# Kernel tuning notes

Hardware: AMD Instinct MI355X
Metric: run time of the kernel (lower is better)

Reference implementation:

```python
import jax, jax.numpy as jnp
import numpy as np

G_NUM, K_DEG = 3, 3  # grid intervals, spline order (module defaults)
LN_EPS = 1e-5


def _bspline_basis(x, grid, k):
    """Cox-de Boor B-spline basis. x: [N, D], grid: [D, G+2k+1] -> [N, D, G+k]."""
    xg = x[:, :, None]                      # [N, D, 1]
    g = grid[None, :, :]                    # [1, D, M]
    B = ((xg >= g[..., :-1]) & (xg < g[..., 1:])).astype(x.dtype)  # degree 0
    for d in range(1, k + 1):
        left = (xg - g[..., :-(d + 1)]) / (g[..., d:-1] - g[..., :-(d + 1)])
        right = (g[..., d + 1:] - xg) / (g[..., d + 1:] - g[..., 1:-d])
        B = left * B[..., :-1] + right * B[..., 1:]
    return B                                # [N, D, G+k]


def _kan_layer(x, grid, coef, scale_base, scale_sp, node_scale, node_bias):
    # spline branch: fold per-edge scale_sp into coef, contract basis without
    # materializing the [N, in, out] per-edge tensor
    basis = _bspline_basis(x, grid, K_DEG)              # [N, in, G+k]
    coef_eff = coef * scale_sp[..., None]               # [in, out, G+k]
    y = jnp.einsum('nib,iob->no', basis, coef_eff)      # spline sum over edges
    y = y + jax.nn.silu(x) @ scale_base                 # residual base function
    return node_scale * y + node_bias                   # per-node affine


def setup_inputs() -> dict:
    key = jax.random.key(0)
    ks = jax.random.split(key, 12)
    B, S = 16, 1024
    D0, D1, D2 = 256, 512, 256
    nb = G_NUM + K_DEG  # num basis fns = 6
    h = 2.0 / G_NUM
    knots = np.arange(-K_DEG, G_NUM + K_DEG + 1) * h - 1.0  # [G+2k+1]=10, range [-3,3]
    grid1 = jnp.asarray(np.tile(knots, (D0, 1)), jnp.float32)
    grid2 = jnp.asarray(np.tile(knots, (D1, 1)), jnp.float32)
    inp = {
        'x': jax.random.normal(ks[0], (B, S, D0), jnp.float32),
        'grid1': grid1,
        'coef1': jax.random.normal(ks[1], (D0, D1, nb), jnp.float32) * 0.1,
        'scale_base1': jax.random.normal(ks[2], (D0, D1), jnp.float32) / np.sqrt(D0),
        'scale_sp1': jnp.ones((D0, D1), jnp.float32),
        'node_scale1': jnp.ones((D1,), jnp.float32),
        'node_bias1': jnp.zeros((D1,), jnp.float32),
        'grid2': grid2,
        'coef2': jax.random.normal(ks[3], (D1, D2, nb), jnp.float32) * 0.1,
        'scale_base2': jax.random.normal(ks[4], (D1, D2), jnp.float32) / np.sqrt(D1),
        'scale_sp2': jnp.ones((D1, D2), jnp.float32),
        'node_scale2': jnp.ones((D2,), jnp.float32),
        'node_bias2': jnp.zeros((D2,), jnp.float32),
        'ln_gamma': jnp.ones((D2,), jnp.float32),
        'ln_beta': jnp.zeros((D2,), jnp.float32),
    }
    return inp


def reference(x, grid1, coef1, scale_base1, scale_sp1, node_scale1, node_bias1,
              grid2, coef2, scale_base2, scale_sp2, node_scale2, node_bias2,
              ln_gamma, ln_beta):
    b, s, d = x.shape
    residual = x  # start_dim == final_dim -> residual path active
    h = x.reshape(-1, d)
    h = _kan_layer(h, grid1, coef1, scale_base1, scale_sp1, node_scale1, node_bias1)
    h = _kan_layer(h, grid2, coef2, scale_base2, scale_sp2, node_scale2, node_bias2)
    h = h.reshape(b, s, -1)
    h = h + residual
    # LayerNorm over last dim
    mu = jnp.mean(h, axis=-1, keepdims=True)
    var = jnp.mean((h - mu) ** 2, axis=-1, keepdims=True)
    h = (h - mu) * jax.lax.rsqrt(var + LN_EPS) * ln_gamma + ln_beta
    # torch nn.GELU default is exact (erf) variant
    return jax.nn.gelu(h, approximate=False)
```

## Files before the change

kernel.cpp:

```cpp
#include <hip/hip_runtime.h>
#include <cstdint>
#include <cstddef>

using f16   = _Float16;
using half4 = __attribute__((ext_vector_type(4))) _Float16;
using half8 = __attribute__((ext_vector_type(8))) _Float16;
using f32x4 = __attribute__((ext_vector_type(4))) float;
using ull   = unsigned long long;

#define DINL __device__ __forceinline__

DINL void gload_lds16(const void* gptr, void* lptr) {
  __builtin_amdgcn_global_load_lds(
      reinterpret_cast<const __attribute__((address_space(1))) uint32_t*>(
          reinterpret_cast<uintptr_t>(gptr)),
      reinterpret_cast<__attribute__((address_space(3))) uint32_t*>(
          reinterpret_cast<uintptr_t>(lptr)),
      16, 0, 0);
}

DINL unsigned pkh(float a, float b) {
  unsigned short ha = __builtin_bit_cast(unsigned short, (f16)a);
  unsigned short hb = __builtin_bit_cast(unsigned short, (f16)b);
  return (unsigned)ha | ((unsigned)hb << 16);
}

struct U4 { unsigned x, y, z, w; };

DINL U4 expand_pack(float x) {
  float xs = (x + 3.0f) * 1.5f;
  float mf = floorf(xs);
  int   m  = (int)mf;
  float u = xs - mf, u2 = u * u, u3 = u2 * u, um = 1.0f - u;
  float p3 = u3 * (1.0f / 6.0f);
  float p2 = (1.0f + 3.0f * (u + u2 - u3)) * (1.0f / 6.0f);
  float p1 = (4.0f - 6.0f * u2 + 3.0f * u3) * (1.0f / 6.0f);
  float p0 = um * um * um * (1.0f / 6.0f);
  ull P = (ull)pkh(p0, p1) | ((ull)pkh(p2, p3) << 32);
  if ((unsigned)m > 8u) P = 0;
  int s    = m * 16 - 48;
  int sneg = min(63, max(0, -s));
  int spos = min(63, max(0, s));
  int shi2 = min(63, max(0, s - 64));
  ull rlo = (s < 0) ? (P >> sneg) : ((s < 64) ? (P << spos) : 0ull);
  ull rhi = (s < 0) ? 0ull
                    : ((s < 64) ? ((P >> (63 - spos)) >> 1) : (P << shi2));
  float sil = x / (1.0f + __expf(-x));
  U4 r;
  r.x = (unsigned)rlo;
  r.y = (unsigned)(rlo >> 32);
  r.z = (unsigned)rhi;
  r.w = pkh(sil, 0.0f);
  return r;
}

__global__ __launch_bounds__(256)
void prep_w_kernel(const float* __restrict__ coef, const float* __restrict__ ssp,
                   const float* __restrict__ sb, f16* __restrict__ Wt,
                   int Din, int Dout) {
  int idx = blockIdx.x * 256 + threadIdx.x;
  if (idx >= Din * Dout) return;
  int n = idx / Din;
  int d = idx - n * Din;
  float s = ssp[(size_t)d * Dout + n];
  const float* c = coef + ((size_t)d * Dout + n) * 6;
  half8 wv;
#pragma unroll
  for (int b = 0; b < 6; ++b) wv[b] = (f16)(c[b] * s);
  wv[6] = (f16)sb[(size_t)d * Dout + n];
  wv[7] = (f16)0.0f;
  int dp = (d & ~7) | ((d & 7) ^ (n & 7));
  *reinterpret_cast<half8*>(Wt + ((size_t)n * Din + dp) * 8) = wv;
}

template <bool BIAS, typename TIN, typename TOUT>
__global__ __launch_bounds__(512, 4)
void kan_gemm(const TIN* __restrict__ X, int ldx,
              const f16* __restrict__ Wt, int ldw,
              const float* __restrict__ nscale, const float* __restrict__ nbias,
              int N, TOUT* __restrict__ Out, int nsteps) {
  __shared__ alignas(16) f16 A0[64 * 64];
  __shared__ alignas(16) f16 A1[64 * 64];
  __shared__ alignas(16) f16 B0[256 * 64];
  __shared__ alignas(16) f16 B1[256 * 64];

  const int tid  = threadIdx.x;
  const int w    = tid >> 6;
  const int lane = tid & 63;
  const int l15  = lane & 15, l7 = lane & 7, hi = lane >> 4;
  const int wm   = w >> 2, wn = w & 3;
  const int m0   = blockIdx.y * 64;
  const int n0   = blockIdx.x * 256;
  const int dim0 = blockIdx.z * (nsteps * 8);
  TOUT* outz = Out + (size_t)blockIdx.z * ((size_t)gridDim.y * 64) * N;

  const int ar = tid >> 3, ad = tid & 7;
  const TIN* asrc = X + (size_t)(m0 + ar) * ldx + dim0 + ad;
  const int aoff = ar * 64 + 8 * (ad ^ (ar & 7));

  const f16* wb[4];
  int ldsb[4];
#pragma unroll
  for (int q = 0; q < 4; ++q) {
    int c   = tid + q * 512;
    wb[q]   = Wt + (size_t)(n0 + (c >> 3)) * ldw + (size_t)dim0 * 8 + (c & 7) * 8;
    ldsb[q] = c * 8;
  }

  f32x4 acc[2][4] = {};

  auto stageB = [&](f16* buf, int k0) {
#pragma unroll
    for (int q = 0; q < 4; ++q) gload_lds16(wb[q] + k0, buf + ldsb[q]);
  };

  auto compute = [&](const f16* bA, const f16* bB) {
    __builtin_amdgcn_s_setprio(1);
#pragma unroll
    for (int kk = 0; kk < 2; ++kk) {
      const int sl = kk * 4 + hi;
      half8 av[2], bv[4];
#pragma unroll
      for (int i = 0; i < 2; ++i)
        av[i] = *reinterpret_cast<const half8*>(
            bA + (wm * 32 + i * 16 + l15) * 64 + 8 * (sl ^ l7));
#pragma unroll
      for (int j = 0; j < 4; ++j)
        bv[j] = *reinterpret_cast<const half8*>(
            bB + (wn * 64 + j * 16 + l15) * 64 + 8 * (sl ^ l7));
#pragma unroll
      for (int i = 0; i < 2; ++i)
#pragma unroll
        for (int j = 0; j < 4; ++j)
          acc[i][j] = __builtin_amdgcn_mfma_f32_16x16x32_f16(av[i], bv[j], acc[i][j], 0, 0, 0);
    }
    __builtin_amdgcn_s_setprio(0);
  };

  auto writeA = [&](f16* buf, U4 e) {
    *reinterpret_cast<U4*>(buf + aoff) = e;
  };

  {
    float xa = (float)asrc[0];
    stageB(B0, 0);
    writeA(A0, expand_pack(xa));
  }
  float xn = (float)asrc[8];
  __syncthreads();

  const TIN* ap = asrc + 16;
  const int npairs = (nsteps - 2) >> 1;
  int k = 64;
  for (int p = 0; p < npairs; ++p) {
    stageB(B1, k);
    float xa2 = (float)ap[0];
    compute(A0, B0);
    writeA(A1, expand_pack(xn));
    __syncthreads();
    stageB(B0, k + 64);
    xn = (float)ap[8];
    compute(A1, B1);
    writeA(A0, expand_pack(xa2));
    __syncthreads();
    ap += 16;
    k  += 128;
  }

  stageB(B1, k);
  compute(A0, B0);
  writeA(A1, expand_pack(xn));
  __syncthreads();
  compute(A1, B1);

#pragma unroll
  for (int j = 0; j < 4; ++j) {
    int col   = n0 + wn * 64 + j * 16 + l15;
    float nsv = nscale[col];
    float nbv = BIAS ? nbias[col] : 0.0f;
#pragma unroll
    for (int i = 0; i < 2; ++i) {
      int rb = m0 + wm * 32 + i * 16 + hi * 4;
#pragma unroll
      for (int r = 0; r < 4; ++r)
        outz[(size_t)(rb + r) * N + col] = (TOUT)(nsv * acc[i][j][r] + nbv);
    }
  }
}

__global__ __launch_bounds__(256)
void ln_gelu_kernel(const f16* __restrict__ P0, const f16* __restrict__ P1,
                    const float* __restrict__ X,  const float* __restrict__ nb2,
                    const float* __restrict__ gamma, const float* __restrict__ beta,
                    float* __restrict__ out, int rows) {
  int row  = blockIdx.x * 4 + (threadIdx.x >> 6);
  int lane = threadIdx.x & 63;
  if (row >= rows) return;
  const half4  a4 = *reinterpret_cast<const half4*>(P0 + (size_t)row * 256 + lane * 4);
  const half4  b4 = *reinterpret_cast<const half4*>(P1 + (size_t)row * 256 + lane * 4);
  const float4 xr = *reinterpret_cast<const float4*>(X  + (size_t)row * 256 + lane * 4);
  const float4 nb = *reinterpret_cast<const float4*>(nb2 + lane * 4);
  const float4 g  = *reinterpret_cast<const float4*>(gamma + lane * 4);
  const float4 be = *reinterpret_cast<const float4*>(beta + lane * 4);
  float h[4];
#pragma unroll
  for (int j = 0; j < 4; ++j)
    h[j] = (float)a4[j] + (float)b4[j] + (&nb.x)[j] + (&xr.x)[j];
  float s = h[0] + h[1] + h[2] + h[3];
#pragma unroll
  for (int o = 32; o >= 1; o >>= 1) s += __shfl_xor(s, o);
  float mu = s * (1.0f / 256.0f);
  float vs = 0.f;
#pragma unroll
  for (int j = 0; j < 4; ++j) { float d = h[j] - mu; vs += d * d; }
#pragma unroll
  for (int o = 32; o >= 1; o >>= 1) vs += __shfl_xor(vs, o);
  float inv = rsqrtf(vs * (1.0f / 256.0f) + 1e-5f);
  float o4[4];
#pragma unroll
  for (int j = 0; j < 4; ++j) {
    float v = (h[j] - mu) * inv * (&g.x)[j] + (&be.x)[j];
    o4[j] = 0.5f * v * (1.0f + erff(v * 0.70710678118654752f));
  }
  *reinterpret_cast<float4*>(out + (size_t)row * 256 + lane * 4) =
      make_float4(o4[0], o4[1], o4[2], o4[3]);
}

extern "C" void kernel_launch(void* const* d_in, const int* in_sizes, int n_in,
                              void* d_out, int out_size, void* d_ws, size_t ws_size,
                              hipStream_t stream) {
  (void)in_sizes; (void)n_in; (void)out_size; (void)ws_size;
  const float* x     = (const float*)d_in[0];
  const float* coef1 = (const float*)d_in[2];
  const float* sb1   = (const float*)d_in[3];
  const float* ssp1  = (const float*)d_in[4];
  const float* ns1   = (const float*)d_in[5];
  const float* nb1   = (const float*)d_in[6];
  const float* coef2 = (const float*)d_in[8];
  const float* sb2   = (const float*)d_in[9];
  const float* ssp2  = (const float*)d_in[10];
  const float* ns2   = (const float*)d_in[11];
  const float* nb2   = (const float*)d_in[12];
  const float* lgam  = (const float*)d_in[13];
  const float* lbet  = (const float*)d_in[14];
  float* out = (float*)d_out;

  const int Ntok = 16 * 1024;
  const int D0 = 256, D1 = 512, D2 = 256;

  char* ws    = (char*)d_ws;
  f16*  h1    = (f16*)ws;
  size_t off  = (size_t)Ntok * D1 * sizeof(f16);
  f16*  part  = (f16*)(ws + off);
  off += (size_t)2 * Ntok * D2 * sizeof(f16);
  f16* Wt1 = (f16*)(ws + off);
  off += (size_t)D1 * D0 * 8 * sizeof(f16);
  f16* Wt2 = (f16*)(ws + off);

  prep_w_kernel<<<(D0 * D1 + 255) / 256, 256, 0, stream>>>(coef1, ssp1, sb1, Wt1, D0, D1);
  prep_w_kernel<<<(D1 * D2 + 255) / 256, 256, 0, stream>>>(coef2, ssp2, sb2, Wt2, D1, D2);

  kan_gemm<true, float, f16><<<dim3(D1 / 256, Ntok / 64, 1), 512, 0, stream>>>(
      x, D0, Wt1, D0 * 8, ns1, nb1, D1, h1, D0 / 8);

  kan_gemm<false, f16, f16><<<dim3(D2 / 256, Ntok / 64, 2), 512, 0, stream>>>(
      h1, D1, Wt2, D1 * 8, ns2, nullptr, D2, part, D1 / 16);

  ln_gelu_kernel<<<Ntok / 4, 256, 0, stream>>>(
      part, part + (size_t)Ntok * D2, x, nb2, lgam, lbet, out, Ntok);
}
```

Before: 118.6 us.

## Load weight fragments directly from global into registers, drop B LDS staging

The GEMM no longer stages weight tiles through LDS via global_load_lds. Each wave now reads its B fragments straight from global memory into registers, with the weight layout left unswizzled to match. Blocks shrink to 4 waves of 256 threads, and each wave covers the full 64 rows and 64 columns (a 4x4 MFMA tile). This cuts LDS use and barrier traffic, but B loads are no longer shared across waves through LDS and their latency is exposed right before the MFMAs with no prefetch.

```diff
diff --git a/kernel.cpp b/kernel.cpp
--- a/kernel.cpp
+++ b/kernel.cpp
@@ -9,15 +9,6 @@
 using ull   = unsigned long long;
 
 #define DINL __device__ __forceinline__
-
-DINL void gload_lds16(const void* gptr, void* lptr) {
-  __builtin_amdgcn_global_load_lds(
-      reinterpret_cast<const __attribute__((address_space(1))) uint32_t*>(
-          reinterpret_cast<uintptr_t>(gptr)),
-      reinterpret_cast<__attribute__((address_space(3))) uint32_t*>(
-          reinterpret_cast<uintptr_t>(lptr)),
-      16, 0, 0);
-}
 
 DINL unsigned pkh(float a, float b) {
   unsigned short ha = __builtin_bit_cast(unsigned short, (f16)a);
@@ -69,118 +60,126 @@
   for (int b = 0; b < 6; ++b) wv[b] = (f16)(c[b] * s);
   wv[6] = (f16)sb[(size_t)d * Dout + n];
   wv[7] = (f16)0.0f;
-  int dp = (d & ~7) | ((d & 7) ^ (n & 7));
-  *reinterpret_cast<half8*>(Wt + ((size_t)n * Din + dp) * 8) = wv;
+  *reinterpret_cast<half8*>(Wt + ((size_t)n * Din + d) * 8) = wv;
 }
 
 template <bool BIAS, typename TIN, typename TOUT>
-__global__ __launch_bounds__(512, 4)
+__global__ __launch_bounds__(256, 2)
 void kan_gemm(const TIN* __restrict__ X, int ldx,
               const f16* __restrict__ Wt, int ldw,
               const float* __restrict__ nscale, const float* __restrict__ nbias,
               int N, TOUT* __restrict__ Out, int nsteps) {
   __shared__ alignas(16) f16 A0[64 * 64];
   __shared__ alignas(16) f16 A1[64 * 64];
-  __shared__ alignas(16) f16 B0[256 * 64];
-  __shared__ alignas(16) f16 B1[256 * 64];
 
   const int tid  = threadIdx.x;
   const int w    = tid >> 6;
   const int lane = tid & 63;
   const int l15  = lane & 15, l7 = lane & 7, hi = lane >> 4;
-  const int wm   = w >> 2, wn = w & 3;
   const int m0   = blockIdx.y * 64;
   const int n0   = blockIdx.x * 256;
   const int dim0 = blockIdx.z * (nsteps * 8);
   TOUT* outz = Out + (size_t)blockIdx.z * ((size_t)gridDim.y * 64) * N;
 
   const int ar = tid >> 3, ad = tid & 7;
-  const TIN* asrc = X + (size_t)(m0 + ar) * ldx + dim0 + ad;
-  const int aoff = ar * 64 + 8 * (ad ^ (ar & 7));
-
-  const f16* wb[4];
-  int ldsb[4];
-#pragma unroll
-  for (int q = 0; q < 4; ++q) {
-    int c   = tid + q * 512;
-    wb[q]   = Wt + (size_t)(n0 + (c >> 3)) * ldw + (size_t)dim0 * 8 + (c & 7) * 8;
-    ldsb[q] = c * 8;
-  }
-
-  f32x4 acc[2][4] = {};
-
-  auto stageB = [&](f16* buf, int k0) {
-#pragma unroll
-    for (int q = 0; q < 4; ++q) gload_lds16(wb[q] + k0, buf + ldsb[q]);
-  };
-
-  auto compute = [&](const f16* bA, const f16* bB) {
+  const TIN* asrc0 = X + (size_t)(m0 + ar) * ldx + dim0 + ad;
+  const TIN* asrc1 = asrc0 + (size_t)32 * ldx;
+  const int aoff0 = ar * 64 + 8 * (ad ^ (ar & 7));
+  const int aoff1 = aoff0 + 32 * 64;
+
+  const f16* bbase = Wt + (size_t)(n0 + w * 64 + l15) * ldw + (size_t)dim0 * 8 + hi * 8;
+  const size_t bj = (size_t)16 * ldw;
+
+  f32x4 acc[4][4] = {};
+
+  auto compute = [&](const f16* bA, const half8* bv) {
     __builtin_amdgcn_s_setprio(1);
 #pragma unroll
     for (int kk = 0; kk < 2; ++kk) {
       const int sl = kk * 4 + hi;
-      half8 av[2], bv[4];
-#pragma unroll
-      for (int i = 0; i < 2; ++i)
+      half8 av[4];
+#pragma unroll
+      for (int i = 0; i < 4; ++i)
         av[i] = *reinterpret_cast<const half8*>(
-            bA + (wm * 32 + i * 16 + l15) * 64 + 8 * (sl ^ l7));
-#pragma unroll
-      for (int j = 0; j < 4; ++j)
-        bv[j] = *reinterpret_cast<const half8*>(
-            bB + (wn * 64 + j * 16 + l15) * 64 + 8 * (sl ^ l7));
-#pragma unroll
-      for (int i = 0; i < 2; ++i)
+            bA + (i * 16 + l15) * 64 + 8 * (sl ^ l7));
+#pragma unroll
+      for (int i = 0; i < 4; ++i)
 #pragma unroll
         for (int j = 0; j < 4; ++j)
-          acc[i][j] = __builtin_amdgcn_mfma_f32_16x16x32_f16(av[i], bv[j], acc[i][j], 0, 0, 0);
+          acc[i][j] = __builtin_amdgcn_mfma_f32_16x16x32_f16(av[i], bv[kk * 4 + j],
+                                                             acc[i][j], 0, 0, 0);
     }
     __builtin_amdgcn_s_setprio(0);
   };
 
-  auto writeA = [&](f16* buf, U4 e) {
-    *reinterpret_cast<U4*>(buf + aoff) = e;
+  auto loadB = [&](int k0, half8* bv) {
+#pragma unroll
+    for (int j = 0; j < 4; ++j) {
+      bv[j]     = *reinterpret_cast<const half8*>(bbase + bj * j + k0);
+      bv[4 + j] = *reinterpret_cast<const half8*>(bbase + bj * j + k0 + 32);
+    }
   };
 
   {
-    float xa = (float)asrc[0];
-    stageB(B0, 0);
-    writeA(A0, expand_pack(xa));
-  }
-  float xn = (float)asrc[8];
+    float xa0 = (float)asrc0[0], xa1 = (float)asrc1[0];
+    U4 e0 = expand_pack(xa0), e1 = expand_pack(xa1);
+    *reinterpret_cast<U4*>(A0 + aoff0) = e0;
+    *reinterpret_cast<U4*>(A0 + aoff1) = e1;
+  }
   __syncthreads();
 
-  const TIN* ap = asrc + 16;
   const int npairs = (nsteps - 2) >> 1;
-  int k = 64;
+  int k  = 0;
+  int kd = 0;
   for (int p = 0; p < npairs; ++p) {
-    stageB(B1, k);
-    float xa2 = (float)ap[0];
-    compute(A0, B0);
-    writeA(A1, expand_pack(xn));
+    {
+      float xn0 = (float)asrc0[kd + 8], xn1 = (float)asrc1[kd + 8];
+      half8 bv[8];
+      loadB(k, bv);
+      compute(A0, bv);
+      U4 e0 = expand_pack(xn0), e1 = expand_pack(xn1);
+      *reinterpret_cast<U4*>(A1 + aoff0) = e0;
+      *reinterpret_cast<U4*>(A1 + aoff1) = e1;
+      __syncthreads();
+    }
+    {
+      float xn0 = (float)asrc0[kd + 16], xn1 = (float)asrc1[kd + 16];
+      half8 bv[8];
+      loadB(k + 64, bv);
+      compute(A1, bv);
+      U4 e0 = expand_pack(xn0), e1 = expand_pack(xn1);
+      *reinterpret_cast<U4*>(A0 + aoff0) = e0;
+      *reinterpret_cast<U4*>(A0 + aoff1) = e1;
+      __syncthreads();
+    }
+    k  += 128;
+    kd += 16;
+  }
+
+  {
+    float xn0 = (float)asrc0[kd + 8], xn1 = (float)asrc1[kd + 8];
+    half8 bv[8];
+    loadB(k, bv);
+    compute(A0, bv);
+    U4 e0 = expand_pack(xn0), e1 = expand_pack(xn1);
+    *reinterpret_cast<U4*>(A1 + aoff0) = e0;
+    *reinterpret_cast<U4*>(A1 + aoff1) = e1;
     __syncthreads();
-    stageB(B0, k + 64);
-    xn = (float)ap[8];
-    compute(A1, B1);
-    writeA(A0, expand_pack(xa2));
-    __syncthreads();
-    ap += 16;
-    k  += 128;
-  }
-
-  stageB(B1, k);
-  compute(A0, B0);
-  writeA(A1, expand_pack(xn));
-  __syncthreads();
-  compute(A1, B1);
+  }
+  {
+    half8 bv[8];
+    loadB(k + 64, bv);
+    compute(A1, bv);
+  }
 
 #pragma unroll
   for (int j = 0; j < 4; ++j) {
-    int col   = n0 + wn * 64 + j * 16 + l15;
+    int col   = n0 + w * 64 + j * 16 + l15;
     float nsv = nscale[col];
     float nbv = BIAS ? nbias[col] : 0.0f;
 #pragma unroll
-    for (int i = 0; i < 2; ++i) {
-      int rb = m0 + wm * 32 + i * 16 + hi * 4;
+    for (int i = 0; i < 4; ++i) {
+      int rb = m0 + i * 16 + hi * 4;
 #pragma unroll
       for (int r = 0; r < 4; ++r)
         outz[(size_t)(rb + r) * N + col] = (TOUT)(nsv * acc[i][j][r] + nbv);
@@ -260,10 +259,10 @@
   prep_w_kernel<<<(D0 * D1 + 255) / 256, 256, 0, stream>>>(coef1, ssp1, sb1, Wt1, D0, D1);
   prep_w_kernel<<<(D1 * D2 + 255) / 256, 256, 0, stream>>>(coef2, ssp2, sb2, Wt2, D1, D2);
 
-  kan_gemm<true, float, f16><<<dim3(D1 / 256, Ntok / 64, 1), 512, 0, stream>>>(
+  kan_gemm<true, float, f16><<<dim3(D1 / 256, Ntok / 64, 1), 256, 0, stream>>>(
       x, D0, Wt1, D0 * 8, ns1, nb1, D1, h1, D0 / 8);
 
-  kan_gemm<false, f16, f16><<<dim3(D2 / 256, Ntok / 64, 2), 512, 0, stream>>>(
+  kan_gemm<false, f16, f16><<<dim3(D2 / 256, Ntok / 64, 2), 256, 0, stream>>>(
       h1, D1, Wt2, D1 * 8, ns2, nullptr, D2, part, D1 / 16);
 
   ln_gelu_kernel<<<Ntok / 4, 256, 0, stream>>>(
```

After: 156.0 us. +31.5%, slower.

## Single-buffer B tile in LDS to raise occupancy of KAN GEMM

Applied to the files above, without the earlier changes.

Replaces the double-buffered 256x64 B tile with one shared buffer, which roughly halves the LDS footprint, and raises the launch-bounds occupancy hint from 4 to 6. Each step now computes, synchronises, loads the next B tile into the same buffer, then synchronises again. The intent is to let more workgroups per CU hide latency across blocks instead of within one block. In exchange, the global-to-LDS load no longer overlaps the MFMA compute inside a block, and each step carries an extra barrier.

```diff
diff --git a/kernel.cpp b/kernel.cpp
--- a/kernel.cpp
+++ b/kernel.cpp
@@ -74,15 +74,14 @@
 }
 
 template <bool BIAS, typename TIN, typename TOUT>
-__global__ __launch_bounds__(512, 4)
+__global__ __launch_bounds__(512, 6)
 void kan_gemm(const TIN* __restrict__ X, int ldx,
               const f16* __restrict__ Wt, int ldw,
               const float* __restrict__ nscale, const float* __restrict__ nbias,
               int N, TOUT* __restrict__ Out, int nsteps) {
   __shared__ alignas(16) f16 A0[64 * 64];
   __shared__ alignas(16) f16 A1[64 * 64];
-  __shared__ alignas(16) f16 B0[256 * 64];
-  __shared__ alignas(16) f16 B1[256 * 64];
+  __shared__ alignas(16) f16 BB[256 * 64];
 
   const int tid  = threadIdx.x;
   const int w    = tid >> 6;
@@ -109,12 +108,12 @@
 
   f32x4 acc[2][4] = {};
 
-  auto stageB = [&](f16* buf, int k0) {
-#pragma unroll
-    for (int q = 0; q < 4; ++q) gload_lds16(wb[q] + k0, buf + ldsb[q]);
+  auto stageB = [&](int k0) {
+#pragma unroll
+    for (int q = 0; q < 4; ++q) gload_lds16(wb[q] + k0, BB + ldsb[q]);
   };
 
-  auto compute = [&](const f16* bA, const f16* bB) {
+  auto compute = [&](const f16* bA) {
     __builtin_amdgcn_s_setprio(1);
 #pragma unroll
     for (int kk = 0; kk < 2; ++kk) {
@@ -127,7 +126,7 @@
 #pragma unroll
       for (int j = 0; j < 4; ++j)
         bv[j] = *reinterpret_cast<const half8*>(
-            bB + (wn * 64 + j * 16 + l15) * 64 + 8 * (sl ^ l7));
+            BB + (wn * 64 + j * 16 + l15) * 64 + 8 * (sl ^ l7));
 #pragma unroll
       for (int i = 0; i < 2; ++i)
 #pragma unroll
@@ -143,35 +142,39 @@
 
   {
     float xa = (float)asrc[0];
-    stageB(B0, 0);
+    stageB(0);
     writeA(A0, expand_pack(xa));
   }
   float xn = (float)asrc[8];
   __syncthreads();
 
-  const TIN* ap = asrc + 16;
   const int npairs = (nsteps - 2) >> 1;
-  int k = 64;
+  int k = 0;
+  int kd = 0;
   for (int p = 0; p < npairs; ++p) {
-    stageB(B1, k);
-    float xa2 = (float)ap[0];
-    compute(A0, B0);
+    float xa2 = (float)asrc[kd + 16];
+    compute(A0);
+    __syncthreads();
+    stageB(k + 64);
     writeA(A1, expand_pack(xn));
     __syncthreads();
-    stageB(B0, k + 64);
-    xn = (float)ap[8];
-    compute(A1, B1);
+    float xb2 = (float)asrc[kd + 24];
+    compute(A1);
+    __syncthreads();
+    stageB(k + 128);
     writeA(A0, expand_pack(xa2));
     __syncthreads();
-    ap += 16;
-    k  += 128;
-  }
-
-  stageB(B1, k);
-  compute(A0, B0);
+    xn = xb2;
+    k += 128;
+    kd += 16;
+  }
+
+  compute(A0);
+  __syncthreads();
+  stageB(k + 64);
   writeA(A1, expand_pack(xn));
   __syncthreads();
-  compute(A1, B1);
+  compute(A1);
 
 #pragma unroll
   for (int j = 0; j < 4; ++j) {
```

Measured after the change: 174.7 us. 1.47x slower.

## Halve GEMM block to 256 threads with 64x64 per-wave output tiles

Applied to the files above, without the earlier changes.

The KAN GEMM block shrinks from 8 waves to 4 waves while keeping the same 64x256 block tile. Each wave now computes a 64x64 sub-tile with a 4x4 accumulator array instead of 32x64, and each thread stages twice as much A and B data into LDS. The aim is more MFMA work per LDS fragment load and fewer threads per barrier. The cost is roughly doubled accumulator registers, fewer waves per CU to hide latency, and an unused leftover variable (bdst).

```diff
diff --git a/kernel.cpp b/kernel.cpp
--- a/kernel.cpp
+++ b/kernel.cpp
@@ -74,7 +74,7 @@
 }
 
 template <bool BIAS, typename TIN, typename TOUT>
-__global__ __launch_bounds__(512, 4)
+__global__ __launch_bounds__(256, 2)
 void kan_gemm(const TIN* __restrict__ X, int ldx,
               const f16* __restrict__ Wt, int ldw,
               const float* __restrict__ nscale, const float* __restrict__ nbias,
@@ -88,30 +88,26 @@
   const int w    = tid >> 6;
   const int lane = tid & 63;
   const int l15  = lane & 15, l7 = lane & 7, hi = lane >> 4;
-  const int wm   = w >> 2, wn = w & 3;
   const int m0   = blockIdx.y * 64;
   const int n0   = blockIdx.x * 256;
   const int dim0 = blockIdx.z * (nsteps * 8);
   TOUT* outz = Out + (size_t)blockIdx.z * ((size_t)gridDim.y * 64) * N;
 
   const int ar = tid >> 3, ad = tid & 7;
-  const TIN* asrc = X + (size_t)(m0 + ar) * ldx + dim0 + ad;
-  const int aoff = ar * 64 + 8 * (ad ^ (ar & 7));
-
-  const f16* wb[4];
-  int ldsb[4];
-#pragma unroll
-  for (int q = 0; q < 4; ++q) {
-    int c   = tid + q * 512;
-    wb[q]   = Wt + (size_t)(n0 + (c >> 3)) * ldw + (size_t)dim0 * 8 + (c & 7) * 8;
-    ldsb[q] = c * 8;
-  }
-
-  f32x4 acc[2][4] = {};
+  const TIN* asrc0 = X + (size_t)(m0 + ar) * ldx + dim0 + ad;
+  const TIN* asrc1 = asrc0 + (size_t)32 * ldx;
+  const int aoff0 = ar * 64 + 8 * (ad ^ (ar & 7));
+  const int aoff1 = aoff0 + 32 * 64;
+
+  const f16* wsrc = Wt + (size_t)(n0 + (tid >> 3)) * ldw + (size_t)dim0 * 8 + (tid & 7) * 8;
+  f16* const bdst = (f16*)nullptr;
+
+  f32x4 acc[4][4] = {};
 
   auto stageB = [&](f16* buf, int k0) {
 #pragma unroll
-    for (int q = 0; q < 4; ++q) gload_lds16(wb[q] + k0, buf + ldsb[q]);
+    for (int q = 0; q < 8; ++q)
+      gload_lds16(wsrc + (size_t)q * 32 * ldw + k0, buf + tid * 8 + q * 2048);
   };
 
   auto compute = [&](const f16* bA, const f16* bB) {
@@ -119,17 +115,17 @@
 #pragma unroll
     for (int kk = 0; kk < 2; ++kk) {
       const int sl = kk * 4 + hi;
-      half8 av[2], bv[4];
-#pragma unroll
-      for (int i = 0; i < 2; ++i)
+      half8 av[4], bv[4];
+#pragma unroll
+      for (int i = 0; i < 4; ++i)
         av[i] = *reinterpret_cast<const half8*>(
-            bA + (wm * 32 + i * 16 + l15) * 64 + 8 * (sl ^ l7));
+            bA + (i * 16 + l15) * 64 + 8 * (sl ^ l7));
 #pragma unroll
       for (int j = 0; j < 4; ++j)
         bv[j] = *reinterpret_cast<const half8*>(
-            bB + (wn * 64 + j * 16 + l15) * 64 + 8 * (sl ^ l7));
-#pragma unroll
-      for (int i = 0; i < 2; ++i)
+            bB + (w * 64 + j * 16 + l15) * 64 + 8 * (sl ^ l7));
+#pragma unroll
+      for (int i = 0; i < 4; ++i)
 #pragma unroll
         for (int j = 0; j < 4; ++j)
           acc[i][j] = __builtin_amdgcn_mfma_f32_16x16x32_f16(av[i], bv[j], acc[i][j], 0, 0, 0);
@@ -137,50 +133,51 @@
     __builtin_amdgcn_s_setprio(0);
   };
 
-  auto writeA = [&](f16* buf, U4 e) {
-    *reinterpret_cast<U4*>(buf + aoff) = e;
+  auto writeA = [&](f16* buf, U4 e0, U4 e1) {
+    *reinterpret_cast<U4*>(buf + aoff0) = e0;
+    *reinterpret_cast<U4*>(buf + aoff1) = e1;
   };
 
   {
-    float xa = (float)asrc[0];
+    float xa0 = (float)asrc0[0], xa1 = (float)asrc1[0];
     stageB(B0, 0);
-    writeA(A0, expand_pack(xa));
-  }
-  float xn = (float)asrc[8];
+    writeA(A0, expand_pack(xa0), expand_pack(xa1));
+  }
+  float xn0 = (float)asrc0[8], xn1 = (float)asrc1[8];
   __syncthreads();
 
-  const TIN* ap = asrc + 16;
   const int npairs = (nsteps - 2) >> 1;
-  int k = 64;
+  int k  = 64;
+  int kd = 16;
   for (int p = 0; p < npairs; ++p) {
     stageB(B1, k);
-    float xa2 = (float)ap[0];
+    float xa0 = (float)asrc0[kd], xa1 = (float)asrc1[kd];
     compute(A0, B0);
-    writeA(A1, expand_pack(xn));
+    writeA(A1, expand_pack(xn0), expand_pack(xn1));
     __syncthreads();
     stageB(B0, k + 64);
-    xn = (float)ap[8];
+    xn0 = (float)asrc0[kd + 8]; xn1 = (float)asrc1[kd + 8];
     compute(A1, B1);
-    writeA(A0, expand_pack(xa2));
+    writeA(A0, expand_pack(xa0), expand_pack(xa1));
     __syncthreads();
-    ap += 16;
     k  += 128;
+    kd += 16;
   }
 
   stageB(B1, k);
   compute(A0, B0);
-  writeA(A1, expand_pack(xn));
+  writeA(A1, expand_pack(xn0), expand_pack(xn1));
   __syncthreads();
   compute(A1, B1);
 
 #pragma unroll
   for (int j = 0; j < 4; ++j) {
-    int col   = n0 + wn * 64 + j * 16 + l15;
+    int col   = n0 + w * 64 + j * 16 + l15;
     float nsv = nscale[col];
     float nbv = BIAS ? nbias[col] : 0.0f;
 #pragma unroll
-    for (int i = 0; i < 2; ++i) {
-      int rb = m0 + wm * 32 + i * 16 + hi * 4;
+    for (int i = 0; i < 4; ++i) {
+      int rb = m0 + i * 16 + hi * 4;
 #pragma unroll
       for (int r = 0; r < 4; ++r)
         outz[(size_t)(rb + r) * N + col] = (TOUT)(nsv * acc[i][j][r] + nbv);
@@ -260,10 +257,10 @@
   prep_w_kernel<<<(D0 * D1 + 255) / 256, 256, 0, stream>>>(coef1, ssp1, sb1, Wt1, D0, D1);
   prep_w_kernel<<<(D1 * D2 + 255) / 256, 256, 0, stream>>>(coef2, ssp2, sb2, Wt2, D1, D2);
 
-  kan_gemm<true, float, f16><<<dim3(D1 / 256, Ntok / 64, 1), 512, 0, stream>>>(
+  kan_gemm<true, float, f16><<<dim3(D1 / 256, Ntok / 64, 1), 256, 0, stream>>>(
       x, D0, Wt1, D0 * 8, ns1, nb1, D1, h1, D0 / 8);
 
-  kan_gemm<false, f16, f16><<<dim3(D2 / 256, Ntok / 64, 2), 512, 0, stream>>>(
+  kan_gemm<false, f16, f16><<<dim3(D2 / 256, Ntok / 64, 2), 256, 0, stream>>>(
       h1, D1, Wt2, D1 * 8, ns2, nullptr, D2, part, D1 / 16);
 
   ln_gelu_kernel<<<Ntok / 4, 256, 0, stream>>>(
```

Measured after the change: 119.7 us. No clear change (+1.0%).
